# Kernel optimization log

Measured on AMD Instinct MI355X. Metric: run time of the kernel, lower is better.

## Reference

```python
import jax, jax.numpy as jnp
import numpy as np


def setup_inputs() -> dict:
    key = jax.random.key(0)
    x = jax.random.normal(key, (4, 4096, 128), dtype=jnp.float32)
    return {"x": x}


def reference(x) -> jnp.ndarray:
    # Unnormalized bilinear self-attention with Q=K=V=x (no softmax).
    # scores[b,t,s] = sum_d x[b,t,d] x[b,s,d]; out[b,t,d] = sum_s scores[b,t,s] x[b,s,d]
    scores = jnp.einsum('btd,bsd->bts', x, x)  # [B,T,T]
    out = jnp.einsum('bts,bsd->btd', scores, x)  # [B,T,D]
    return out
```

## Files before the change

### kernel.cpp

```cpp
#include <hip/hip_runtime.h>

#define BATCH 4
#define T 4096
#define D 128
#define CHUNKS 64
#define ROWS1 64
#define ROWS2 64
#define S2 136

typedef __attribute__((ext_vector_type(4))) float f32x4;
typedef __attribute__((ext_vector_type(8))) short bf16x8;

__device__ __forceinline__ unsigned short f2b(float f) {
    unsigned u = __builtin_bit_cast(unsigned, f);
    u += 0x7FFFu + ((u >> 16) & 1u);
    return (unsigned short)(u >> 16);
}

__global__ __launch_bounds__(256) void k_partial_g(const float* __restrict__ x,
                                                   float* __restrict__ part) {
    __shared__ float Xs[ROWS1 * D];
    const int blk = blockIdx.x;
    const int b = blk / CHUNKS, chunk = blk % CHUNKS;
    const float* xp = x + ((size_t)b * T + (size_t)chunk * ROWS1) * D;
    const int tid = threadIdx.x;

    const float4* xp4 = (const float4*)xp;
    float4* Xs4 = (float4*)Xs;
    #pragma unroll
    for (int i = 0; i < (ROWS1 * D / 4) / 256; i++)
        Xs4[tid + i * 256] = xp4[tid + i * 256];
    __syncthreads();

    const int ty = tid >> 4, tx = tid & 15;
    const int r0 = ty * 8;
    const int c0 = tx * 4;

    float acc[8][8];
    #pragma unroll
    for (int i = 0; i < 8; i++)
        #pragma unroll
        for (int j = 0; j < 8; j++) acc[i][j] = 0.f;

    for (int t = 0; t < ROWS1; t++) {
        const float* row = Xs + t * D;
        float a[8], bv[8];
        #pragma unroll
        for (int i = 0; i < 8; i++) a[i] = row[r0 + i];
        #pragma unroll
        for (int j = 0; j < 4; j++) { bv[j] = row[c0 + j]; bv[4 + j] = row[64 + c0 + j]; }
        #pragma unroll
        for (int i = 0; i < 8; i++)
            #pragma unroll
            for (int j = 0; j < 8; j++) acc[i][j] += a[i] * bv[j];
    }

    float* pp = part + (size_t)blk * (D * D);
    #pragma unroll
    for (int i = 0; i < 8; i++) {
        *(float4*)(pp + (r0 + i) * D + c0)      = make_float4(acc[i][0], acc[i][1], acc[i][2], acc[i][3]);
        *(float4*)(pp + (r0 + i) * D + 64 + c0) = make_float4(acc[i][4], acc[i][5], acc[i][6], acc[i][7]);
    }
}

__global__ __launch_bounds__(256) void k_reduce_g(const float* __restrict__ part,
                                                  unsigned short* __restrict__ g) {
    const int o = blockIdx.x * 256 + threadIdx.x;
    const int b = o >> 14;
    const int e = o & 16383;
    const float* p = part + ((size_t)b * CHUNKS) * (D * D) + e;
    float s[8];
    #pragma unroll
    for (int i = 0; i < 8; i++) s[i] = 0.f;
    for (int c = 0; c < CHUNKS; c += 8) {
        #pragma unroll
        for (int i = 0; i < 8; i++)
            s[i] += p[(size_t)(c + i) * (D * D)];
    }
    float sum = ((s[0] + s[1]) + (s[2] + s[3])) + ((s[4] + s[5]) + (s[6] + s[7]));
    g[o] = f2b(sum);
}

__global__ __launch_bounds__(256) void k_xg_mfma(const float* __restrict__ x,
                                                 const unsigned short* __restrict__ g,
                                                 float* __restrict__ out) {
    __shared__ unsigned short Xs[ROWS2 * S2];
    __shared__ unsigned short Gs[D * S2];
    const int blk = blockIdx.x;
    const int b = blk >> 6, chunk = blk & 63;
    const float* xp = x + ((size_t)b * T + (size_t)chunk * ROWS2) * D;
    const unsigned short* gp = g + (size_t)b * (D * D);
    const int tid = threadIdx.x;

    {
        const int dg = tid & 31, tr = tid >> 5;
        #pragma unroll
        for (int ii = 0; ii < 8; ii++) {
            const int t = tr + ii * 8;
            float4 v = ((const float4*)(xp + t * D))[dg];
            ushort4 pk;
            pk.x = f2b(v.x); pk.y = f2b(v.y); pk.z = f2b(v.z); pk.w = f2b(v.w);
            *(ushort4*)(Xs + t * S2 + dg * 4) = pk;
        }
    }
    {
        const int f4 = tid & 15, r = tid >> 4;
        #pragma unroll
        for (int ii = 0; ii < 8; ii++) {
            const int row = r + ii * 16;
            uint4 gv = ((const uint4*)(gp + row * D))[f4];
            *(uint4*)(Gs + row * S2 + f4 * 8) = gv;
        }
    }
    __syncthreads();

    const int lane = tid & 63, w = tid >> 6;
    const int m = lane & 15, q = lane >> 4;

    f32x4 acc[8];
    #pragma unroll
    for (int ni = 0; ni < 8; ni++) acc[ni] = (f32x4){0.f, 0.f, 0.f, 0.f};

    const unsigned short* arow = Xs + (w * 16 + m) * S2 + q * 8;
    const unsigned short* brow = Gs + m * S2 + q * 8;

    #pragma unroll
    for (int s = 0; s < 4; s++) {
        bf16x8 a = *(const bf16x8*)(arow + s * 32);
        #pragma unroll
        for (int ni = 0; ni < 8; ni++) {
            bf16x8 bb = *(const bf16x8*)(brow + ni * 16 * S2 + s * 32);
            acc[ni] = __builtin_amdgcn_mfma_f32_16x16x32_bf16(a, bb, acc[ni], 0, 0, 0);
        }
    }

    float* op = out + ((size_t)b * T + (size_t)chunk * ROWS2) * D;
    const int row0 = w * 16 + q * 4;
    #pragma unroll
    for (int ni = 0; ni < 8; ni++)
        #pragma unroll
        for (int r = 0; r < 4; r++)
            op[(row0 + r) * D + ni * 16 + m] = acc[ni][r];
}

extern "C" void kernel_launch(void* const* d_in, const int* in_sizes, int n_in,
                              void* d_out, int out_size, void* d_ws, size_t ws_size,
                              hipStream_t stream) {
    const float* x = (const float*)d_in[0];
    float* out = (float*)d_out;

    const size_t part_elems = (size_t)BATCH * CHUNKS * D * D;
    float* part = (float*)d_ws;
    unsigned short* g = (unsigned short*)(part + part_elems);

    k_partial_g<<<BATCH * CHUNKS, 256, 0, stream>>>(x, part);
    k_reduce_g<<<BATCH * D * D / 256, 256, 0, stream>>>(part, g);
    k_xg_mfma<<<BATCH * 64, 256, 0, stream>>>(x, g, out);
}
```

Measured before the change: 78.64 us.

## Compute partial Gram matrices with bf16 MFMA and store partials as bf16

Replaces the scalar FP32 outer-product partial Gram kernel with a bf16 MFMA version that transposes the x chunk into LDS. Partial Gram results are written as bf16 instead of fp32, which halves the partial buffer traffic read back by the reduction kernel. In exchange, precision drops because x is rounded to bf16 and each of the 64 partial sums is rounded before accumulation.

```diff
diff --git a/kernel.cpp b/kernel.cpp
--- a/kernel.cpp
+++ b/kernel.cpp
@@ -6,6 +6,7 @@
 #define CHUNKS 64
 #define ROWS1 64
 #define ROWS2 64
+#define ST1 72
 #define S2 136
 
 typedef __attribute__((ext_vector_type(4))) float f32x4;
@@ -16,66 +17,85 @@
     u += 0x7FFFu + ((u >> 16) & 1u);
     return (unsigned short)(u >> 16);
 }
+__device__ __forceinline__ float b2f(unsigned short h) {
+    return __builtin_bit_cast(float, (unsigned)h << 16);
+}
 
-__global__ __launch_bounds__(256) void k_partial_g(const float* __restrict__ x,
-                                                   float* __restrict__ part) {
-    __shared__ float Xs[ROWS1 * D];
+__global__ __launch_bounds__(256) void k_gram(const float* __restrict__ x,
+                                              unsigned short* __restrict__ part) {
+    __shared__ unsigned short XT[D * ST1];
     const int blk = blockIdx.x;
-    const int b = blk / CHUNKS, chunk = blk % CHUNKS;
+    const int b = blk >> 6, chunk = blk & 63;
     const float* xp = x + ((size_t)b * T + (size_t)chunk * ROWS1) * D;
     const int tid = threadIdx.x;
 
-    const float4* xp4 = (const float4*)xp;
-    float4* Xs4 = (float4*)Xs;
     #pragma unroll
-    for (int i = 0; i < (ROWS1 * D / 4) / 256; i++)
-        Xs4[tid + i * 256] = xp4[tid + i * 256];
+    for (int pass = 0; pass < 8; pass++) {
+        const int slot = (tid >> 6) + 4 * pass;
+        const int dd = 2 * (tid & 7) + 16 * (slot & 7);
+        const int tpg = ((tid >> 3) & 7) + 8 * (slot >> 3);
+        const int t = 2 * tpg;
+        float2 f0 = *(const float2*)(xp + (size_t)t * D + dd);
+        float2 f1 = *(const float2*)(xp + (size_t)(t + 1) * D + dd);
+        unsigned u0 = (unsigned)f2b(f0.x) | ((unsigned)f2b(f1.x) << 16);
+        unsigned u1 = (unsigned)f2b(f0.y) | ((unsigned)f2b(f1.y) << 16);
+        *(unsigned*)(XT + dd * ST1 + 2 * tpg) = u0;
+        *(unsigned*)(XT + (dd + 1) * ST1 + 2 * tpg) = u1;
+    }
     __syncthreads();
 
-    const int ty = tid >> 4, tx = tid & 15;
-    const int r0 = ty * 8;
-    const int c0 = tx * 4;
+    const int lane = tid & 63, w = tid >> 6;
+    const int m = lane & 15, q = lane >> 4;
+    const int m0 = w * 32;
 
-    float acc[8][8];
+    f32x4 acc[2][8];
     #pragma unroll
-    for (int i = 0; i < 8; i++)
+    for (int mi = 0; mi < 2; mi++)
         #pragma unroll
-        for (int j = 0; j < 8; j++) acc[i][j] = 0.f;
+        for (int ni = 0; ni < 8; ni++) acc[mi][ni] = (f32x4){0.f, 0.f, 0.f, 0.f};
 
-    for (int t = 0; t < ROWS1; t++) {
-        const float* row = Xs + t * D;
-        float a[8], bv[8];
+    #pragma unroll
+    for (int s = 0; s < 2; s++) {
+        bf16x8 av[2], bv[8];
         #pragma unroll
-        for (int i = 0; i < 8; i++) a[i] = row[r0 + i];
+        for (int mi = 0; mi < 2; mi++)
+            av[mi] = *(const bf16x8*)(XT + (m0 + mi * 16 + m) * ST1 + q * 8 + s * 32);
         #pragma unroll
-        for (int j = 0; j < 4; j++) { bv[j] = row[c0 + j]; bv[4 + j] = row[64 + c0 + j]; }
+        for (int ni = 0; ni < 8; ni++)
+            bv[ni] = *(const bf16x8*)(XT + (ni * 16 + m) * ST1 + q * 8 + s * 32);
         #pragma unroll
-        for (int i = 0; i < 8; i++)
+        for (int mi = 0; mi < 2; mi++)
             #pragma unroll
-            for (int j = 0; j < 8; j++) acc[i][j] += a[i] * bv[j];
+            for (int ni = 0; ni < 8; ni++)
+                acc[mi][ni] = __builtin_amdgcn_mfma_f32_16x16x32_bf16(av[mi], bv[ni], acc[mi][ni], 0, 0, 0);
     }
 
-    float* pp = part + (size_t)blk * (D * D);
+    unsigned short* pp = part + (size_t)blk * (D * D);
     #pragma unroll
-    for (int i = 0; i < 8; i++) {
-        *(float4*)(pp + (r0 + i) * D + c0)      = make_float4(acc[i][0], acc[i][1], acc[i][2], acc[i][3]);
-        *(float4*)(pp + (r0 + i) * D + 64 + c0) = make_float4(acc[i][4], acc[i][5], acc[i][6], acc[i][7]);
-    }
+    for (int mi = 0; mi < 2; mi++)
+        #pragma unroll
+        for (int ni = 0; ni < 8; ni++) {
+            const int row0 = m0 + mi * 16 + q * 4;
+            const int col = ni * 16 + m;
+            #pragma unroll
+            for (int r = 0; r < 4; r++)
+                pp[(size_t)(row0 + r) * D + col] = f2b(acc[mi][ni][r]);
+        }
 }
 
-__global__ __launch_bounds__(256) void k_reduce_g(const float* __restrict__ part,
+__global__ __launch_bounds__(256) void k_reduce_g(const unsigned short* __restrict__ part,
                                                   unsigned short* __restrict__ g) {
     const int o = blockIdx.x * 256 + threadIdx.x;
     const int b = o >> 14;
     const int e = o & 16383;
-    const float* p = part + ((size_t)b * CHUNKS) * (D * D) + e;
+    const unsigned short* p = part + ((size_t)b * CHUNKS) * (D * D) + e;
     float s[8];
     #pragma unroll
     for (int i = 0; i < 8; i++) s[i] = 0.f;
     for (int c = 0; c < CHUNKS; c += 8) {
         #pragma unroll
         for (int i = 0; i < 8; i++)
-            s[i] += p[(size_t)(c + i) * (D * D)];
+            s[i] += b2f(p[(size_t)(c + i) * (D * D)]);
     }
     float sum = ((s[0] + s[1]) + (s[2] + s[3])) + ((s[4] + s[5]) + (s[6] + s[7]));
     g[o] = f2b(sum);
@@ -150,10 +170,10 @@
     float* out = (float*)d_out;
 
     const size_t part_elems = (size_t)BATCH * CHUNKS * D * D;
-    float* part = (float*)d_ws;
-    unsigned short* g = (unsigned short*)(part + part_elems);
+    unsigned short* part = (unsigned short*)d_ws;
+    unsigned short* g = part + part_elems;
 
-    k_partial_g<<<BATCH * CHUNKS, 256, 0, stream>>>(x, part);
+    k_gram<<<BATCH * CHUNKS, 256, 0, stream>>>(x, part);
     k_reduce_g<<<BATCH * D * D / 256, 256, 0, stream>>>(part, g);
     k_xg_mfma<<<BATCH * 64, 256, 0, stream>>>(x, g, out);
 }
```

Result: faster. 68.87 us (-12.4%).
